# Optimization experiments

Hardware: AMD Instinct MI355X
Metric: run time of the kernel (lower is better)

## Reference

```python
import jax, jax.numpy as jnp
import numpy as np

N = 50000      # nodes
E = 800000     # edges (avg in-degree 16)
IN_DIM = 128
OUT_DIM = 64
LEAKY_SLOPE = 0.01  # torch F.leaky_relu default


def setup_inputs() -> dict:
    key = jax.random.key(0)
    ks = jax.random.split(key, 7)
    h = jax.random.normal(ks[0], (N, IN_DIM), dtype=jnp.float32)
    r_h = jax.random.normal(ks[1], (E, OUT_DIM), dtype=jnp.float32)
    edge_src = jax.random.randint(ks[2], (E,), 0, N, dtype=jnp.int32)
    edge_dst = jax.random.randint(ks[3], (E,), 0, N, dtype=jnp.int32)
    # learned params (xavier-ish scaling)
    W_fc = jax.random.normal(ks[4], (OUT_DIM, IN_DIM), dtype=jnp.float32) * (1.0 / np.sqrt(IN_DIM))
    attn_w = jax.random.normal(ks[5], (1, 3 * OUT_DIM), dtype=jnp.float32) * 0.1
    loop_weight = jax.random.normal(ks[6], (OUT_DIM, OUT_DIM), dtype=jnp.float32) * (1.0 / np.sqrt(OUT_DIM))
    return {"h": h, "r_h": r_h, "W_fc": W_fc, "attn_w": attn_w,
            "loop_weight": loop_weight, "edge_src": edge_src, "edge_dst": edge_dst}


def reference(h, r_h, W_fc, attn_w, loop_weight, edge_src, edge_dst):
    # z = fc(h)   [N, OUT_DIM]
    z = h @ W_fc.T
    z_src = z[edge_src]          # [E, OUT_DIM]
    z_dst = z[edge_dst]          # [E, OUT_DIM]
    # attn_fc(cat([z_src, z_dst, r_h])) expressed without materializing the concat
    w1 = attn_w[0, :OUT_DIM]
    w2 = attn_w[0, OUT_DIM:2 * OUT_DIM]
    w3 = attn_w[0, 2 * OUT_DIM:]
    a = z_src @ w1 + z_dst @ w2 + r_h @ w3            # [E]
    e = jax.nn.leaky_relu(a, LEAKY_SLOPE)
    # segment softmax over incoming edges of each destination node
    seg_max = jax.ops.segment_max(e, edge_dst, num_segments=N)  # -inf for deg-0 (never gathered)
    e_exp = jnp.exp(e - jax.lax.stop_gradient(seg_max)[edge_dst])
    denom = jax.ops.segment_sum(e_exp, edge_dst, num_segments=N)
    alpha = e_exp / denom[edge_dst]                   # [E]
    # weighted scatter-sum of source features
    agg = jax.ops.segment_sum(alpha[:, None] * z_src, edge_dst, num_segments=N)  # [N, OUT_DIM]
    # DGL only runs reduce_func (incl. self-loop matmul) on nodes with in-edges
    deg = jax.ops.segment_sum(jnp.ones((E,), jnp.float32), edge_dst, num_segments=N)
    h_out = jnp.where(deg[:, None] > 0, agg + z @ loop_weight, 0.0)
    return jax.nn.relu(h_out)
```

## Files before the change

### kernel.cpp

```cpp
#include <hip/hip_runtime.h>
#include <hip/hip_bf16.h>

#define NN 50000
#define EE 800000
#define IND 128
#define OUTD 64
#define NB 49
#define PA_BLOCKS 782
#define DEG_BLOCKS 391
#define RH_BLOCKS 6250

__global__ __launch_bounds__(256) void k_stream(
    const float* __restrict__ attn, const int* __restrict__ edst,
    const float* __restrict__ r_h, int* __restrict__ deg,
    int* __restrict__ rank, float* __restrict__ d3) {
  const int tid = threadIdx.x;
  if (blockIdx.x < DEG_BLOCKS) {
    const int base = blockIdx.x * 2048 + tid;
#pragma unroll
    for (int j = 0; j < 8; ++j) {
      int e = base + j * 256;
      if (e < EE) rank[e] = atomicAdd(&deg[edst[e]], 1);
    }
    return;
  }
  const int base4 = (blockIdx.x - DEG_BLOCKS) * 2048 + tid;
  const int sub = tid & 15;
  const float4 wv = reinterpret_cast<const float4*>(attn + 2 * OUTD)[sub];
  float4 rv[8];
#pragma unroll
  for (int j = 0; j < 8; ++j)
    rv[j] = reinterpret_cast<const float4*>(r_h)[base4 + j * 256];
  float d[8];
#pragma unroll
  for (int j = 0; j < 8; ++j)
    d[j] = rv[j].x * wv.x + rv[j].y * wv.y + rv[j].z * wv.z + rv[j].w * wv.w;
#pragma unroll
  for (int m = 1; m <= 8; m <<= 1) {
#pragma unroll
    for (int j = 0; j < 8; ++j) d[j] += __shfl_xor(d[j], m, 64);
  }
  if (sub == 0) {
    const int row0 = base4 >> 4;
#pragma unroll
    for (int j = 0; j < 8; ++j) d3[row0 + 16 * j] = d[j];
  }
}

__global__ __launch_bounds__(256, 1) void k_gemm(
    const float* __restrict__ h, const float* __restrict__ W,
    const float* __restrict__ attn, __hip_bfloat16* __restrict__ zb,
    float* __restrict__ s1, float* __restrict__ s2) {
  const int tid = threadIdx.x;
  __shared__ float Wl[64 * 129];
#pragma unroll
  for (int j = 0; j < 8; ++j) {
    int i4 = tid + j * 256;
    const float4 v = reinterpret_cast<const float4*>(W)[i4];
    int i = i4 * 4;
    int col = i >> 7, k = i & 127;
    float* p = &Wl[col * 129 + k];
    p[0] = v.x; p[1] = v.y; p[2] = v.z; p[3] = v.w;
  }
  __syncthreads();
  const int lane = tid & 63;
  const int wid = tid >> 6;
  float Wreg[128];
#pragma unroll
  for (int k = 0; k < 128; ++k) Wreg[k] = Wl[lane * 129 + k];
  const float w1v = attn[lane];
  const float w2v = attn[64 + lane];
  const int base = blockIdx.x * 64 + wid * 16;
  int rmax = NN - base;
  rmax = rmax > 16 ? 16 : (rmax < 0 ? 0 : rmax);
  for (int i = 0; i < rmax; ++i) {
    int r = base + i;
    const float* hr = h + (size_t)r * IND;
    float h0 = hr[lane];
    float h1 = hr[64 + lane];
    float a0 = 0.f, a1 = 0.f, a2 = 0.f, a3 = 0.f;
#pragma unroll
    for (int k = 0; k < 16; ++k) {
      a0 = fmaf(__uint_as_float(__builtin_amdgcn_readlane(__float_as_uint(h0), 4 * k)),     Wreg[4 * k], a0);
      a1 = fmaf(__uint_as_float(__builtin_amdgcn_readlane(__float_as_uint(h0), 4 * k + 1)), Wreg[4 * k + 1], a1);
      a2 = fmaf(__uint_as_float(__builtin_amdgcn_readlane(__float_as_uint(h0), 4 * k + 2)), Wreg[4 * k + 2], a2);
      a3 = fmaf(__uint_as_float(__builtin_amdgcn_readlane(__float_as_uint(h0), 4 * k + 3)), Wreg[4 * k + 3], a3);
    }
#pragma unroll
    for (int k = 0; k < 16; ++k) {
      a0 = fmaf(__uint_as_float(__builtin_amdgcn_readlane(__float_as_uint(h1), 4 * k)),     Wreg[64 + 4 * k], a0);
      a1 = fmaf(__uint_as_float(__builtin_amdgcn_readlane(__float_as_uint(h1), 4 * k + 1)), Wreg[64 + 4 * k + 1], a1);
      a2 = fmaf(__uint_as_float(__builtin_amdgcn_readlane(__float_as_uint(h1), 4 * k + 2)), Wreg[64 + 4 * k + 2], a2);
      a3 = fmaf(__uint_as_float(__builtin_amdgcn_readlane(__float_as_uint(h1), 4 * k + 3)), Wreg[64 + 4 * k + 3], a3);
    }
    float acc = (a0 + a1) + (a2 + a3);
    zb[(size_t)r * OUTD + lane] = __float2bfloat16(acc);
    float p = acc * w1v, q = acc * w2v;
#pragma unroll
    for (int m = 32; m >= 1; m >>= 1) {
      p += __shfl_xor(p, m, 64);
      q += __shfl_xor(q, m, 64);
    }
    if (lane == 0) { s1[r] = p; s2[r] = q; }
  }
}

__global__ __launch_bounds__(1024) void k_scan1(
    const int* __restrict__ deg, int* __restrict__ offL,
    int* __restrict__ blocksum) {
  __shared__ int wsum[16];
  __shared__ int woff[17];
  const int tid = threadIdx.x;
  const int gid = blockIdx.x * 1024 + tid;
  const int lane = tid & 63, wid = tid >> 6;
  int v = (gid < NN) ? deg[gid] : 0;
  int incl = v;
#pragma unroll
  for (int o = 1; o < 64; o <<= 1) {
    int t = __shfl_up(incl, o, 64);
    if (lane >= o) incl += t;
  }
  if (lane == 63) wsum[wid] = incl;
  __syncthreads();
  if (wid == 0 && lane < 16) {
    int s = wsum[lane];
    int si = s;
#pragma unroll
    for (int o = 1; o < 16; o <<= 1) {
      int t = __shfl_up(si, o, 64);
      if (lane >= o) si += t;
    }
    woff[lane] = si - s;
    if (lane == 15) woff[16] = si;
  }
  __syncthreads();
  if (gid < NN) offL[gid] = woff[wid] + incl - v;
  if (tid == 0) blocksum[blockIdx.x] = woff[16];
}

__global__ __launch_bounds__(64) void k_scan2(
    const int* __restrict__ blocksum, int* __restrict__ blockoff) {
  const int lane = threadIdx.x;
  int v = (lane < NB) ? blocksum[lane] : 0;
  int incl = v;
#pragma unroll
  for (int o = 1; o < 64; o <<= 1) {
    int t = __shfl_up(incl, o, 64);
    if (lane >= o) incl += t;
  }
  if (lane < NB) blockoff[lane] = incl - v;
}

__global__ __launch_bounds__(256) void k_scatter(
    const int* __restrict__ esrc, const int* __restrict__ edst,
    const float* __restrict__ d3, const float* __restrict__ s1,
    const float* __restrict__ s2, const int* __restrict__ rank,
    const int* __restrict__ offL, const int* __restrict__ blockoff,
    int2* __restrict__ pairs) {
  const int t = blockIdx.x * 256 + threadIdx.x;
  if (t >= EE / 4) return;
  const int4 s4 = reinterpret_cast<const int4*>(esrc)[t];
  const int4 dd4 = reinterpret_cast<const int4*>(edst)[t];
  const float4 d34 = reinterpret_cast<const float4*>(d3)[t];
  const int4 rk4 = reinterpret_cast<const int4*>(rank)[t];
  float v1x = s1[s4.x], v1y = s1[s4.y], v1z = s1[s4.z], v1w = s1[s4.w];
  float v2x = s2[dd4.x], v2y = s2[dd4.y], v2z = s2[dd4.z], v2w = s2[dd4.w];
  int oLx = offL[dd4.x], oLy = offL[dd4.y], oLz = offL[dd4.z], oLw = offL[dd4.w];
  int bx = blockoff[dd4.x >> 10], by = blockoff[dd4.y >> 10];
  int bz = blockoff[dd4.z >> 10], bw = blockoff[dd4.w >> 10];
  float ax = v1x + v2x + d34.x, ay = v1y + v2y + d34.y;
  float az = v1z + v2z + d34.z, aw = v1w + v2w + d34.w;
  float ex = __expf(ax > 0.f ? ax : 0.01f * ax);
  float ey = __expf(ay > 0.f ? ay : 0.01f * ay);
  float ez = __expf(az > 0.f ? az : 0.01f * az);
  float ew = __expf(aw > 0.f ? aw : 0.01f * aw);
  pairs[bx + oLx + rk4.x] = make_int2(s4.x, __float_as_int(ex));
  pairs[by + oLy + rk4.y] = make_int2(s4.y, __float_as_int(ey));
  pairs[bz + oLz + rk4.z] = make_int2(s4.z, __float_as_int(ez));
  pairs[bw + oLw + rk4.w] = make_int2(s4.w, __float_as_int(ew));
}

__global__ __launch_bounds__(256) void k_agg(
    const __hip_bfloat16* __restrict__ zb, const int2* __restrict__ pairs,
    const int* __restrict__ offL, const int* __restrict__ blockoff,
    const int* __restrict__ deg, const float* __restrict__ LW,
    float* __restrict__ out) {
  const int lane = threadIdx.x & 63, wid = threadIdx.x >> 6;
  const int slot = lane >> 4, sub = lane & 15;
  float4 LWreg[16];
#pragma unroll
  for (int kl = 0; kl < 16; ++kl)
    LWreg[kl] = reinterpret_cast<const float4*>(LW)[(slot * 16 + kl) * 16 + sub];
  const int r = blockIdx.x * 4 + wid;
  const int cnt = deg[r];
  const int2* pp = pairs + (blockoff[r >> 10] + offL[r]);
  float4 acc = make_float4(0.f, 0.f, 0.f, 0.f);
  float wsum = 0.f;
  for (int i = 0; i < cnt; i += 16) {
    int2 p[4];
    float w[4];
#pragma unroll
    for (int j = 0; j < 4; ++j) {
      int e = i + j * 4 + slot;
      bool v = e < cnt;
      p[j] = pp[v ? e : 0];
      w[j] = v ? __int_as_float(p[j].y) : 0.f;
    }
#pragma unroll
    for (int j = 0; j < 4; ++j) {
      ushort4 uz = reinterpret_cast<const ushort4*>(zb)[(size_t)p[j].x * 16 + sub];
      acc.x = fmaf(w[j], __uint_as_float((unsigned)uz.x << 16), acc.x);
      acc.y = fmaf(w[j], __uint_as_float((unsigned)uz.y << 16), acc.y);
      acc.z = fmaf(w[j], __uint_as_float((unsigned)uz.z << 16), acc.z);
      acc.w = fmaf(w[j], __uint_as_float((unsigned)uz.w << 16), acc.w);
      wsum += w[j];
    }
  }
  float4 lacc = make_float4(0.f, 0.f, 0.f, 0.f);
#pragma unroll
  for (int j = 0; j < 4; ++j) {
    ushort4 uz = reinterpret_cast<const ushort4*>(zb)[(size_t)r * 16 + slot * 4 + j];
    float zk[4] = {__uint_as_float((unsigned)uz.x << 16),
                   __uint_as_float((unsigned)uz.y << 16),
                   __uint_as_float((unsigned)uz.z << 16),
                   __uint_as_float((unsigned)uz.w << 16)};
#pragma unroll
    for (int c = 0; c < 4; ++c) {
      float4 lw = LWreg[4 * j + c];
      lacc.x = fmaf(zk[c], lw.x, lacc.x);
      lacc.y = fmaf(zk[c], lw.y, lacc.y);
      lacc.z = fmaf(zk[c], lw.z, lacc.z);
      lacc.w = fmaf(zk[c], lw.w, lacc.w);
    }
  }
  wsum += __shfl_xor(wsum, 16, 64);
  wsum += __shfl_xor(wsum, 32, 64);
  float inv = (cnt > 0) ? 1.f / wsum : 0.f;
  float4 t;
  t.x = fmaf(acc.x, inv, lacc.x);
  t.y = fmaf(acc.y, inv, lacc.y);
  t.z = fmaf(acc.z, inv, lacc.z);
  t.w = fmaf(acc.w, inv, lacc.w);
  t.x += __shfl_xor(t.x, 16, 64); t.x += __shfl_xor(t.x, 32, 64);
  t.y += __shfl_xor(t.y, 16, 64); t.y += __shfl_xor(t.y, 32, 64);
  t.z += __shfl_xor(t.z, 16, 64); t.z += __shfl_xor(t.z, 32, 64);
  t.w += __shfl_xor(t.w, 16, 64); t.w += __shfl_xor(t.w, 32, 64);
  if (slot == 0) {
    float4 res;
    res.x = (cnt > 0 && t.x > 0.f) ? t.x : 0.f;
    res.y = (cnt > 0 && t.y > 0.f) ? t.y : 0.f;
    res.z = (cnt > 0 && t.z > 0.f) ? t.z : 0.f;
    res.w = (cnt > 0 && t.w > 0.f) ? t.w : 0.f;
    reinterpret_cast<float4*>(out)[(size_t)r * 16 + sub] = res;
  }
}

extern "C" void kernel_launch(void* const* d_in, const int* in_sizes, int n_in,
                              void* d_out, int out_size, void* d_ws, size_t ws_size,
                              hipStream_t stream) {
  const float* h    = (const float*)d_in[0];
  const float* r_h  = (const float*)d_in[1];
  const float* W_fc = (const float*)d_in[2];
  const float* attn = (const float*)d_in[3];
  const float* LW   = (const float*)d_in[4];
  const int* esrc   = (const int*)d_in[5];
  const int* edst   = (const int*)d_in[6];
  float* out = (float*)d_out;

  char* ws = (char*)d_ws;
  __hip_bfloat16* zb = (__hip_bfloat16*)(ws);
  int2*  pairs = (int2*)(ws + 6400000);
  int*   rank  = (int*)(ws + 12800000);
  float* d3    = (float*)(ws + 16000000);
  float* s1    = (float*)(ws + 19200000);
  float* s2    = (float*)(ws + 19400000);
  int*   deg   = (int*)(ws + 19600000);
  int*   offL  = (int*)(ws + 19800000);
  int*   bsum  = (int*)(ws + 20000000);
  int*   boff  = (int*)(ws + 20001024);

  hipMemsetAsync(deg, 0, (size_t)NN * sizeof(int), stream);

  k_stream<<<DEG_BLOCKS + RH_BLOCKS, 256, 0, stream>>>(
      attn, edst, r_h, deg, rank, d3);
  k_gemm<<<PA_BLOCKS, 256, 0, stream>>>(h, W_fc, attn, zb, s1, s2);
  k_scan1<<<NB, 1024, 0, stream>>>(deg, offL, bsum);
  k_scan2<<<1, 64, 0, stream>>>(bsum, boff);
  k_scatter<<<(EE / 4 + 255) / 256, 256, 0, stream>>>(
      esrc, edst, d3, s1, s2, rank, offL, boff, pairs);
  k_agg<<<NN / 4, 256, 0, stream>>>(zb, pairs, offL, boff, deg, LW, out);
}
```

Measured before the change: 424.9 us.

## Fuse r_h attention dot into scatter and replace rank array with atomic cursors

The r_h·w3 dot product moves out of the streaming kernel into the scatter kernel, so the d3 intermediate is no longer written and read back. The per-edge rank array from the degree pass is dropped. Slots are now claimed in scatter with a second per-node atomic counter (cur), which adds atomics but removes the rank traffic. Edge order within a segment becomes nondeterministic, and k_gemm's launch bounds are relaxed to allow two blocks per CU.

```diff
diff --git a/kernel.cpp b/kernel.cpp
--- a/kernel.cpp
+++ b/kernel.cpp
@@ -8,46 +8,18 @@
 #define NB 49
 #define PA_BLOCKS 782
 #define DEG_BLOCKS 391
-#define RH_BLOCKS 6250
-
-__global__ __launch_bounds__(256) void k_stream(
-    const float* __restrict__ attn, const int* __restrict__ edst,
-    const float* __restrict__ r_h, int* __restrict__ deg,
-    int* __restrict__ rank, float* __restrict__ d3) {
-  const int tid = threadIdx.x;
-  if (blockIdx.x < DEG_BLOCKS) {
-    const int base = blockIdx.x * 2048 + tid;
-#pragma unroll
-    for (int j = 0; j < 8; ++j) {
-      int e = base + j * 256;
-      if (e < EE) rank[e] = atomicAdd(&deg[edst[e]], 1);
-    }
-    return;
-  }
-  const int base4 = (blockIdx.x - DEG_BLOCKS) * 2048 + tid;
-  const int sub = tid & 15;
-  const float4 wv = reinterpret_cast<const float4*>(attn + 2 * OUTD)[sub];
-  float4 rv[8];
-#pragma unroll
-  for (int j = 0; j < 8; ++j)
-    rv[j] = reinterpret_cast<const float4*>(r_h)[base4 + j * 256];
-  float d[8];
-#pragma unroll
-  for (int j = 0; j < 8; ++j)
-    d[j] = rv[j].x * wv.x + rv[j].y * wv.y + rv[j].z * wv.z + rv[j].w * wv.w;
-#pragma unroll
-  for (int m = 1; m <= 8; m <<= 1) {
-#pragma unroll
-    for (int j = 0; j < 8; ++j) d[j] += __shfl_xor(d[j], m, 64);
-  }
-  if (sub == 0) {
-    const int row0 = base4 >> 4;
-#pragma unroll
-    for (int j = 0; j < 8; ++j) d3[row0 + 16 * j] = d[j];
-  }
-}
-
-__global__ __launch_bounds__(256, 1) void k_gemm(
+
+__global__ __launch_bounds__(256) void k_deg(
+    const int* __restrict__ edst, int* __restrict__ deg) {
+  const int base = blockIdx.x * 2048 + threadIdx.x;
+#pragma unroll
+  for (int j = 0; j < 8; ++j) {
+    int e = base + j * 256;
+    if (e < EE) atomicAdd(&deg[edst[e]], 1);
+  }
+}
+
+__global__ __launch_bounds__(256, 2) void k_gemm(
     const float* __restrict__ h, const float* __restrict__ W,
     const float* __restrict__ attn, __hip_bfloat16* __restrict__ zb,
     float* __restrict__ s1, float* __restrict__ s2) {
@@ -153,31 +125,46 @@
 
 __global__ __launch_bounds__(256) void k_scatter(
     const int* __restrict__ esrc, const int* __restrict__ edst,
-    const float* __restrict__ d3, const float* __restrict__ s1,
-    const float* __restrict__ s2, const int* __restrict__ rank,
+    const float* __restrict__ r_h, const float* __restrict__ attn,
+    const float* __restrict__ s1, const float* __restrict__ s2,
     const int* __restrict__ offL, const int* __restrict__ blockoff,
-    int2* __restrict__ pairs) {
-  const int t = blockIdx.x * 256 + threadIdx.x;
-  if (t >= EE / 4) return;
-  const int4 s4 = reinterpret_cast<const int4*>(esrc)[t];
-  const int4 dd4 = reinterpret_cast<const int4*>(edst)[t];
-  const float4 d34 = reinterpret_cast<const float4*>(d3)[t];
-  const int4 rk4 = reinterpret_cast<const int4*>(rank)[t];
-  float v1x = s1[s4.x], v1y = s1[s4.y], v1z = s1[s4.z], v1w = s1[s4.w];
-  float v2x = s2[dd4.x], v2y = s2[dd4.y], v2z = s2[dd4.z], v2w = s2[dd4.w];
-  int oLx = offL[dd4.x], oLy = offL[dd4.y], oLz = offL[dd4.z], oLw = offL[dd4.w];
-  int bx = blockoff[dd4.x >> 10], by = blockoff[dd4.y >> 10];
-  int bz = blockoff[dd4.z >> 10], bw = blockoff[dd4.w >> 10];
-  float ax = v1x + v2x + d34.x, ay = v1y + v2y + d34.y;
-  float az = v1z + v2z + d34.z, aw = v1w + v2w + d34.w;
-  float ex = __expf(ax > 0.f ? ax : 0.01f * ax);
-  float ey = __expf(ay > 0.f ? ay : 0.01f * ay);
-  float ez = __expf(az > 0.f ? az : 0.01f * az);
-  float ew = __expf(aw > 0.f ? aw : 0.01f * aw);
-  pairs[bx + oLx + rk4.x] = make_int2(s4.x, __float_as_int(ex));
-  pairs[by + oLy + rk4.y] = make_int2(s4.y, __float_as_int(ey));
-  pairs[bz + oLz + rk4.z] = make_int2(s4.z, __float_as_int(ez));
-  pairs[bw + oLw + rk4.w] = make_int2(s4.w, __float_as_int(ew));
+    int* __restrict__ cur, int2* __restrict__ pairs) {
+  const int tid = threadIdx.x;
+  const int g = tid >> 4, sub = tid & 15;
+  const int e0 = blockIdx.x * 64 + g * 4;
+  const float4 wv = reinterpret_cast<const float4*>(attn + 2 * OUTD)[sub];
+  float4 rv[4];
+#pragma unroll
+  for (int j = 0; j < 4; ++j)
+    rv[j] = reinterpret_cast<const float4*>(r_h)[(size_t)(e0 + j) * 16 + sub];
+  float d[4];
+#pragma unroll
+  for (int j = 0; j < 4; ++j)
+    d[j] = rv[j].x * wv.x + rv[j].y * wv.y + rv[j].z * wv.z + rv[j].w * wv.w;
+#pragma unroll
+  for (int m = 1; m <= 8; m <<= 1) {
+#pragma unroll
+    for (int j = 0; j < 4; ++j) d[j] += __shfl_xor(d[j], m, 64);
+  }
+  if (sub == 0) {
+    const int4 s4  = *reinterpret_cast<const int4*>(esrc + e0);
+    const int4 dd4 = *reinterpret_cast<const int4*>(edst + e0);
+    float v1x = s1[s4.x], v1y = s1[s4.y], v1z = s1[s4.z], v1w = s1[s4.w];
+    float v2x = s2[dd4.x], v2y = s2[dd4.y], v2z = s2[dd4.z], v2w = s2[dd4.w];
+    int oLx = offL[dd4.x], oLy = offL[dd4.y], oLz = offL[dd4.z], oLw = offL[dd4.w];
+    int bx = blockoff[dd4.x >> 10], by = blockoff[dd4.y >> 10];
+    int bz = blockoff[dd4.z >> 10], bw = blockoff[dd4.w >> 10];
+    float ax = v1x + v2x + d[0], ay = v1y + v2y + d[1];
+    float az = v1z + v2z + d[2], aw = v1w + v2w + d[3];
+    float ex = __expf(ax > 0.f ? ax : 0.01f * ax);
+    float ey = __expf(ay > 0.f ? ay : 0.01f * ay);
+    float ez = __expf(az > 0.f ? az : 0.01f * az);
+    float ew = __expf(aw > 0.f ? aw : 0.01f * aw);
+    pairs[bx + oLx + atomicAdd(&cur[dd4.x], 1)] = make_int2(s4.x, __float_as_int(ex));
+    pairs[by + oLy + atomicAdd(&cur[dd4.y], 1)] = make_int2(s4.y, __float_as_int(ey));
+    pairs[bz + oLz + atomicAdd(&cur[dd4.z], 1)] = make_int2(s4.z, __float_as_int(ez));
+    pairs[bw + oLw + atomicAdd(&cur[dd4.w], 1)] = make_int2(s4.w, __float_as_int(ew));
+  }
 }
 
 __global__ __launch_bounds__(256) void k_agg(
@@ -270,23 +257,21 @@
   char* ws = (char*)d_ws;
   __hip_bfloat16* zb = (__hip_bfloat16*)(ws);
   int2*  pairs = (int2*)(ws + 6400000);
-  int*   rank  = (int*)(ws + 12800000);
-  float* d3    = (float*)(ws + 16000000);
-  float* s1    = (float*)(ws + 19200000);
-  float* s2    = (float*)(ws + 19400000);
-  int*   deg   = (int*)(ws + 19600000);
-  int*   offL  = (int*)(ws + 19800000);
-  int*   bsum  = (int*)(ws + 20000000);
-  int*   boff  = (int*)(ws + 20001024);
-
-  hipMemsetAsync(deg, 0, (size_t)NN * sizeof(int), stream);
-
-  k_stream<<<DEG_BLOCKS + RH_BLOCKS, 256, 0, stream>>>(
-      attn, edst, r_h, deg, rank, d3);
+  float* s1    = (float*)(ws + 12800000);
+  float* s2    = (float*)(ws + 13000000);
+  int*   deg   = (int*)(ws + 13200000);
+  int*   cur   = (int*)(ws + 13400000);
+  int*   offL  = (int*)(ws + 13600000);
+  int*   bsum  = (int*)(ws + 13800000);
+  int*   boff  = (int*)(ws + 13801024);
+
+  hipMemsetAsync(ws + 13200000, 0, 400000, stream);
+
+  k_deg<<<DEG_BLOCKS, 256, 0, stream>>>(edst, deg);
   k_gemm<<<PA_BLOCKS, 256, 0, stream>>>(h, W_fc, attn, zb, s1, s2);
   k_scan1<<<NB, 1024, 0, stream>>>(deg, offL, bsum);
   k_scan2<<<1, 64, 0, stream>>>(bsum, boff);
-  k_scatter<<<(EE / 4 + 255) / 256, 256, 0, stream>>>(
-      esrc, edst, d3, s1, s2, rank, offL, boff, pairs);
+  k_scatter<<<EE / 64, 256, 0, stream>>>(
+      esrc, edst, r_h, attn, s1, s2, offL, boff, cur, pairs);
   k_agg<<<NN / 4, 256, 0, stream>>>(zb, pairs, offL, boff, deg, LW, out);
 }
```

Result: slower. 448.3 us (+5.5%).

## Merge GEMM and streaming kernels; fold block-offset scan into consumers

Applied to the files above, without the earlier changes.

Combines the z GEMM with the degree-count and r_h dot-product streaming work into one launch, using blockIdx ranges to pick the role. This removes a launch and lets the independent phases overlap. The second-level scan kernel is dropped, and each k_scatter and k_agg block recomputes the 49-entry block-offset prefix sum into shared memory. That costs a small redundant scan and a __syncthreads per block. The merged kernel carries __launch_bounds__(256,1) for every block role, which may limit occupancy for the streaming blocks.

```diff
diff --git a/kernel.cpp b/kernel.cpp
--- a/kernel.cpp
+++ b/kernel.cpp
@@ -10,13 +10,40 @@
 #define DEG_BLOCKS 391
 #define RH_BLOCKS 6250
 
-__global__ __launch_bounds__(256) void k_stream(
+__global__ __launch_bounds__(256, 1) void k_front(
+    const float* __restrict__ h, const float* __restrict__ W,
     const float* __restrict__ attn, const int* __restrict__ edst,
-    const float* __restrict__ r_h, int* __restrict__ deg,
-    int* __restrict__ rank, float* __restrict__ d3) {
+    const float* __restrict__ r_h,
+    __hip_bfloat16* __restrict__ zb, float* __restrict__ s1,
+    float* __restrict__ s2, int* __restrict__ deg, int* __restrict__ rank,
+    float* __restrict__ d3) {
   const int tid = threadIdx.x;
-  if (blockIdx.x < DEG_BLOCKS) {
-    const int base = blockIdx.x * 2048 + tid;
+  if (blockIdx.x >= PA_BLOCKS + DEG_BLOCKS) {
+    const int base4 = (blockIdx.x - (PA_BLOCKS + DEG_BLOCKS)) * 2048 + tid;
+    const int sub = tid & 15;
+    const float4 wv = reinterpret_cast<const float4*>(attn + 2 * OUTD)[sub];
+    float4 rv[8];
+#pragma unroll
+    for (int j = 0; j < 8; ++j)
+      rv[j] = reinterpret_cast<const float4*>(r_h)[base4 + j * 256];
+    float d[8];
+#pragma unroll
+    for (int j = 0; j < 8; ++j)
+      d[j] = rv[j].x * wv.x + rv[j].y * wv.y + rv[j].z * wv.z + rv[j].w * wv.w;
+#pragma unroll
+    for (int m = 1; m <= 8; m <<= 1) {
+#pragma unroll
+      for (int j = 0; j < 8; ++j) d[j] += __shfl_xor(d[j], m, 64);
+    }
+    if (sub == 0) {
+      const int row0 = base4 >> 4;
+#pragma unroll
+      for (int j = 0; j < 8; ++j) d3[row0 + 16 * j] = d[j];
+    }
+    return;
+  }
+  if (blockIdx.x >= PA_BLOCKS) {
+    const int base = (blockIdx.x - PA_BLOCKS) * 2048 + tid;
 #pragma unroll
     for (int j = 0; j < 8; ++j) {
       int e = base + j * 256;
@@ -24,34 +51,6 @@
     }
     return;
   }
-  const int base4 = (blockIdx.x - DEG_BLOCKS) * 2048 + tid;
-  const int sub = tid & 15;
-  const float4 wv = reinterpret_cast<const float4*>(attn + 2 * OUTD)[sub];
-  float4 rv[8];
-#pragma unroll
-  for (int j = 0; j < 8; ++j)
-    rv[j] = reinterpret_cast<const float4*>(r_h)[base4 + j * 256];
-  float d[8];
-#pragma unroll
-  for (int j = 0; j < 8; ++j)
-    d[j] = rv[j].x * wv.x + rv[j].y * wv.y + rv[j].z * wv.z + rv[j].w * wv.w;
-#pragma unroll
-  for (int m = 1; m <= 8; m <<= 1) {
-#pragma unroll
-    for (int j = 0; j < 8; ++j) d[j] += __shfl_xor(d[j], m, 64);
-  }
-  if (sub == 0) {
-    const int row0 = base4 >> 4;
-#pragma unroll
-    for (int j = 0; j < 8; ++j) d3[row0 + 16 * j] = d[j];
-  }
-}
-
-__global__ __launch_bounds__(256, 1) void k_gemm(
-    const float* __restrict__ h, const float* __restrict__ W,
-    const float* __restrict__ attn, __hip_bfloat16* __restrict__ zb,
-    float* __restrict__ s1, float* __restrict__ s2) {
-  const int tid = threadIdx.x;
   __shared__ float Wl[64 * 129];
 #pragma unroll
   for (int j = 0; j < 8; ++j) {
@@ -138,25 +137,25 @@
   if (tid == 0) blocksum[blockIdx.x] = woff[16];
 }
 
-__global__ __launch_bounds__(64) void k_scan2(
-    const int* __restrict__ blocksum, int* __restrict__ blockoff) {
-  const int lane = threadIdx.x;
-  int v = (lane < NB) ? blocksum[lane] : 0;
-  int incl = v;
-#pragma unroll
-  for (int o = 1; o < 64; o <<= 1) {
-    int t = __shfl_up(incl, o, 64);
-    if (lane >= o) incl += t;
-  }
-  if (lane < NB) blockoff[lane] = incl - v;
-}
-
 __global__ __launch_bounds__(256) void k_scatter(
     const int* __restrict__ esrc, const int* __restrict__ edst,
     const float* __restrict__ d3, const float* __restrict__ s1,
     const float* __restrict__ s2, const int* __restrict__ rank,
-    const int* __restrict__ offL, const int* __restrict__ blockoff,
+    const int* __restrict__ offL, const int* __restrict__ bsum,
     int2* __restrict__ pairs) {
+  __shared__ int boffs[NB];
+  if (threadIdx.x < 64) {
+    int l = threadIdx.x;
+    int v = (l < NB) ? bsum[l] : 0;
+    int incl = v;
+#pragma unroll
+    for (int o = 1; o < 64; o <<= 1) {
+      int t = __shfl_up(incl, o, 64);
+      if (l >= o) incl += t;
+    }
+    if (l < NB) boffs[l] = incl - v;
+  }
+  __syncthreads();
   const int t = blockIdx.x * 256 + threadIdx.x;
   if (t >= EE / 4) return;
   const int4 s4 = reinterpret_cast<const int4*>(esrc)[t];
@@ -166,8 +165,8 @@
   float v1x = s1[s4.x], v1y = s1[s4.y], v1z = s1[s4.z], v1w = s1[s4.w];
   float v2x = s2[dd4.x], v2y = s2[dd4.y], v2z = s2[dd4.z], v2w = s2[dd4.w];
   int oLx = offL[dd4.x], oLy = offL[dd4.y], oLz = offL[dd4.z], oLw = offL[dd4.w];
-  int bx = blockoff[dd4.x >> 10], by = blockoff[dd4.y >> 10];
-  int bz = blockoff[dd4.z >> 10], bw = blockoff[dd4.w >> 10];
+  int bx = boffs[dd4.x >> 10], by = boffs[dd4.y >> 10];
+  int bz = boffs[dd4.z >> 10], bw = boffs[dd4.w >> 10];
   float ax = v1x + v2x + d34.x, ay = v1y + v2y + d34.y;
   float az = v1z + v2z + d34.z, aw = v1w + v2w + d34.w;
   float ex = __expf(ax > 0.f ? ax : 0.01f * ax);
@@ -182,9 +181,22 @@
 
 __global__ __launch_bounds__(256) void k_agg(
     const __hip_bfloat16* __restrict__ zb, const int2* __restrict__ pairs,
-    const int* __restrict__ offL, const int* __restrict__ blockoff,
+    const int* __restrict__ offL, const int* __restrict__ bsum,
     const int* __restrict__ deg, const float* __restrict__ LW,
     float* __restrict__ out) {
+  __shared__ int boffs[NB];
+  if (threadIdx.x < 64) {
+    int l = threadIdx.x;
+    int v = (l < NB) ? bsum[l] : 0;
+    int incl = v;
+#pragma unroll
+    for (int o = 1; o < 64; o <<= 1) {
+      int t = __shfl_up(incl, o, 64);
+      if (l >= o) incl += t;
+    }
+    if (l < NB) boffs[l] = incl - v;
+  }
+  __syncthreads();
   const int lane = threadIdx.x & 63, wid = threadIdx.x >> 6;
   const int slot = lane >> 4, sub = lane & 15;
   float4 LWreg[16];
@@ -193,7 +205,7 @@
     LWreg[kl] = reinterpret_cast<const float4*>(LW)[(slot * 16 + kl) * 16 + sub];
   const int r = blockIdx.x * 4 + wid;
   const int cnt = deg[r];
-  const int2* pp = pairs + (blockoff[r >> 10] + offL[r]);
+  const int2* pp = pairs + (boffs[r >> 10] + offL[r]);
   float4 acc = make_float4(0.f, 0.f, 0.f, 0.f);
   float wsum = 0.f;
   for (int i = 0; i < cnt; i += 16) {
@@ -277,16 +289,13 @@
   int*   deg   = (int*)(ws + 19600000);
   int*   offL  = (int*)(ws + 19800000);
   int*   bsum  = (int*)(ws + 20000000);
-  int*   boff  = (int*)(ws + 20001024);
 
   hipMemsetAsync(deg, 0, (size_t)NN * sizeof(int), stream);
 
-  k_stream<<<DEG_BLOCKS + RH_BLOCKS, 256, 0, stream>>>(
-      attn, edst, r_h, deg, rank, d3);
-  k_gemm<<<PA_BLOCKS, 256, 0, stream>>>(h, W_fc, attn, zb, s1, s2);
+  k_front<<<PA_BLOCKS + DEG_BLOCKS + RH_BLOCKS, 256, 0, stream>>>(
+      h, W_fc, attn, edst, r_h, zb, s1, s2, deg, rank, d3);
   k_scan1<<<NB, 1024, 0, stream>>>(deg, offL, bsum);
-  k_scan2<<<1, 64, 0, stream>>>(bsum, boff);
   k_scatter<<<(EE / 4 + 255) / 256, 256, 0, stream>>>(
-      esrc, edst, d3, s1, s2, rank, offL, boff, pairs);
-  k_agg<<<NN / 4, 256, 0, stream>>>(zb, pairs, offL, boff, deg, LW, out);
-}
+      esrc, edst, d3, s1, s2, rank, offL, bsum, pairs);
+  k_agg<<<NN / 4, 256, 0, stream>>>(zb, pairs, offL, bsum, deg, LW, out);
+}
```

After: 424.6 us. No clear change (-0.1%).
